# Kernel tuning notes

Measured on AMD Instinct MI355X. Metric: run time of the kernel, lower is better.

The kernel has to match this reference:

```python
import jax, jax.numpy as jnp
import numpy as np
from math import sqrt

N_HEADS = 8

def setup_inputs() -> dict:
    key = jax.random.key(0)
    k1, k2, k3 = jax.random.split(key, 3)
    B, S, D = 2, 2048, 512
    X = jax.random.normal(k1, (B, S, D), dtype=jnp.float32)
    # kaiming_normal for (fan_in = D) -> std = sqrt(2/D)
    Wq = jax.random.normal(k2, (D, D), dtype=jnp.float32) * jnp.float32(sqrt(2.0 / D))
    Wv = jax.random.normal(k3, (D, 1), dtype=jnp.float32) * jnp.float32(sqrt(2.0 / D))
    return {"X": X, "Wq": Wq, "Wv": Wv}

def reference(X, Wq, Wv):
    B, S, D = X.shape
    H = N_HEADS
    dh = D // H
    # Q: (B, H, S, dh)
    Q = (X @ Wq).reshape(B, S, H, dh).transpose(0, 2, 1, 3)
    # NOTE: original uses L2 norm (NOT squared) in the 'distance' expression; be faithful.
    n = jnp.linalg.norm(Q, axis=-1, keepdims=True)          # (B,H,S,1)
    dots = jnp.einsum('bhsd,bhtd->bhst', Q, Q)              # (B,H,S,S)
    scores = -(n - 2.0 * dots + jnp.swapaxes(n, -2, -1)) / jnp.float32(sqrt(dh))
    P = jax.nn.softmax(scores, axis=-1)                     # (B,H,S,S)
    # Wh: (H, D, dh); Ah = Wh @ Wh^T : (H, D, D)
    Wh = Wq.reshape(D, H, dh).transpose(1, 0, 2)
    Ah = jnp.einsum('hij,hkj->hik', Wh, Wh)
    PX = jnp.einsum('bhst,btd->bhsd', P, X)                 # (B,H,S,D)
    attn_scores = jnp.einsum('bhsd,hde->bhse', PX, Ah)      # (B,H,S,D)
    applied = attn_scores @ Wv                              # (B,H,S,1)
    # GumbelSigmoid in eval mode (deterministic): plain sigmoid of logits.
    selection = jax.nn.sigmoid(applied)
    return selection
```

## Files before the change

### kernel.cpp

```cpp
#include <hip/hip_runtime.h>


typedef __attribute__((ext_vector_type(8))) short bf16x8;
typedef __attribute__((ext_vector_type(4))) float f32x4;

#if __has_builtin(__builtin_amdgcn_exp2f)
#define EXP2F(x) __builtin_amdgcn_exp2f(x)
#else
#define EXP2F(x) exp2f(x)
#endif

#define LOG2E 1.44269504088896341f
#define C025  (0.25f * LOG2E)
#define C0125 (0.125f * LOG2E)

__device__ inline unsigned int f2b(float f) {
    unsigned int u = __float_as_uint(f);
    return (u + 0x7fffu + ((u >> 16) & 1u)) >> 16;
}

#define SWZ(row, c) ((row) * 64 + (((c) ^ ((row) & 7)) * 8))

__global__ __launch_bounds__(256) void qgemm_k(const float* __restrict__ X,
                                               const float* __restrict__ Wq,
                                               const float* __restrict__ Wv,
                                               unsigned short* __restrict__ Qh,
                                               float* __restrict__ n_out,
                                               float* __restrict__ y_out) {
    __shared__ __align__(16) unsigned short As[64 * 64];
    __shared__ __align__(16) unsigned short Bs[64 * 64];
    __shared__ float tsh[256];
    int tid = threadIdx.x;
    int h = blockIdx.x;
    int m0 = blockIdx.y * 64;
    int n0 = h * 64;
    int w = tid >> 6, lane = tid & 63;
    int tt = lane & 15, quad = lane >> 4;

    int arow = tid >> 3, achk = tid & 7;
    int bc = tid & 63, bjg = tid >> 6;

    const float* Xa0 = &X[(m0 + arow) * 512 + achk * 8];
    const float* Xa1 = Xa0 + 32 * 512;
    const float* Wb  = &Wq[n0 + bc];

    float4 a00, a01, a10, a11;
    float bv[16], wv[16];
    float tp = 0.f;
    f32x4 acc[4] = {{0.f,0.f,0.f,0.f},{0.f,0.f,0.f,0.f},
                    {0.f,0.f,0.f,0.f},{0.f,0.f,0.f,0.f}};

#define K1_LOADS(K0)                                                     \
    do {                                                                 \
        a00 = *(const float4*)&Xa0[(K0)];                                \
        a01 = *(const float4*)&Xa0[(K0) + 4];                            \
        a10 = *(const float4*)&Xa1[(K0)];                                \
        a11 = *(const float4*)&Xa1[(K0) + 4];                            \
        _Pragma("unroll")                                                \
        for (int i = 0; i < 8; ++i) {                                    \
            bv[i]     = Wb[((K0) + bjg * 8 + i) * 512];                  \
            bv[8 + i] = Wb[((K0) + (bjg + 4) * 8 + i) * 512];            \
            wv[i]     = Wv[(K0) + bjg * 8 + i];                          \
            wv[8 + i] = Wv[(K0) + (bjg + 4) * 8 + i];                    \
        }                                                                \
    } while (0)

    K1_LOADS(0);
    for (int k0 = 0; k0 < 512; k0 += 64) {
        __syncthreads();
        uint4 o;
        o.x = f2b(a00.x) | (f2b(a00.y) << 16);
        o.y = f2b(a00.z) | (f2b(a00.w) << 16);
        o.z = f2b(a01.x) | (f2b(a01.y) << 16);
        o.w = f2b(a01.z) | (f2b(a01.w) << 16);
        *(uint4*)&As[SWZ(arow, achk)] = o;
        o.x = f2b(a10.x) | (f2b(a10.y) << 16);
        o.y = f2b(a10.z) | (f2b(a10.w) << 16);
        o.z = f2b(a11.x) | (f2b(a11.y) << 16);
        o.w = f2b(a11.z) | (f2b(a11.w) << 16);
        *(uint4*)&As[SWZ(arow + 32, achk)] = o;
        o.x = f2b(bv[0]) | (f2b(bv[1]) << 16);
        o.y = f2b(bv[2]) | (f2b(bv[3]) << 16);
        o.z = f2b(bv[4]) | (f2b(bv[5]) << 16);
        o.w = f2b(bv[6]) | (f2b(bv[7]) << 16);
        *(uint4*)&Bs[SWZ(bc, bjg)] = o;
        o.x = f2b(bv[8])  | (f2b(bv[9])  << 16);
        o.y = f2b(bv[10]) | (f2b(bv[11]) << 16);
        o.z = f2b(bv[12]) | (f2b(bv[13]) << 16);
        o.w = f2b(bv[14]) | (f2b(bv[15]) << 16);
        *(uint4*)&Bs[SWZ(bc, bjg + 4)] = o;
        #pragma unroll
        for (int i = 0; i < 16; ++i) tp = fmaf(bv[i], wv[i], tp);
        __syncthreads();
        if (k0 < 448) K1_LOADS(k0 + 64);
        int ar = w * 16 + tt;
        bf16x8 fa0 = *(const bf16x8*)&As[SWZ(ar, quad)];
        bf16x8 fa1 = *(const bf16x8*)&As[SWZ(ar, quad + 4)];
        #pragma unroll
        for (int ct = 0; ct < 4; ++ct) {
            int br = ct * 16 + tt;
            bf16x8 fb0 = *(const bf16x8*)&Bs[SWZ(br, quad)];
            bf16x8 fb1 = *(const bf16x8*)&Bs[SWZ(br, quad + 4)];
            acc[ct] = __builtin_amdgcn_mfma_f32_16x16x32_bf16(fa0, fb0, acc[ct], 0, 0, 0);
            acc[ct] = __builtin_amdgcn_mfma_f32_16x16x32_bf16(fa1, fb1, acc[ct], 0, 0, 0);
        }
    }

    tsh[bjg * 64 + bc] = tp;
    __syncthreads();
    float tv[4];
    #pragma unroll
    for (int ct = 0; ct < 4; ++ct) {
        int c = ct * 16 + tt;
        tv[ct] = tsh[c] + tsh[64 + c] + tsh[128 + c] + tsh[192 + c];
    }

    float s2[4] = {0.f,0.f,0.f,0.f}, yp[4] = {0.f,0.f,0.f,0.f};
    #pragma unroll
    for (int ct = 0; ct < 4; ++ct)
        #pragma unroll
        for (int g = 0; g < 4; ++g) {
            float v = acc[ct][g];
            s2[g] = fmaf(v, v, s2[g]);
            yp[g] = fmaf(v, tv[ct], yp[g]);
            Qh[(m0 + w * 16 + quad * 4 + g) * 512 + n0 + ct * 16 + tt] =
                (unsigned short)f2b(v);
        }
    #pragma unroll
    for (int off = 1; off <= 8; off <<= 1)
        #pragma unroll
        for (int g = 0; g < 4; ++g) {
            s2[g] += __shfl_xor(s2[g], off);
            yp[g] += __shfl_xor(yp[g], off);
        }
    if (tt == 0) {
        int bb = m0 >> 11;
        #pragma unroll
        for (int g = 0; g < 4; ++g) {
            int row = m0 + w * 16 + quad * 4 + g;
            int idx = ((bb * 8 + h) << 11) + (row & 2047);
            n_out[idx] = sqrtf(s2[g]);
            y_out[idx] = yp[g];
        }
    }
}

__global__ __launch_bounds__(512, 4) void attn_k(const unsigned short* __restrict__ Qh,
                                                 const float* __restrict__ n_in,
                                                 const float* __restrict__ y_in,
                                                 float* __restrict__ out) {
    __shared__ float redN[8][64];
    __shared__ float redD[8][64];
    int tid = threadIdx.x;
    int bh = blockIdx.x >> 5;
    int tile = blockIdx.x & 31;
    int s0 = tile * 64;
    int b = bh >> 3, h = bh & 7;
    const unsigned short* Qb = Qh + (size_t)(b * 2048) * 512 + h * 64;
    const float* nb = n_in + bh * 2048;
    const float* yb = y_in + bh * 2048;
    int w = tid >> 6, lane = tid & 63;
    int tt = lane & 15, quad = lane >> 4;

    bf16x8 fa0[4], fa1[4];
    #pragma unroll
    for (int tl = 0; tl < 4; ++tl) {
        const unsigned short* r = &Qb[(size_t)(s0 + tl * 16 + tt) * 512];
        fa0[tl] = *(const bf16x8*)&r[quad * 8];
        fa1[tl] = *(const bf16x8*)&r[32 + quad * 8];
    }
    f32x4 num[4] = {{0.f,0.f,0.f,0.f},{0.f,0.f,0.f,0.f},
                    {0.f,0.f,0.f,0.f},{0.f,0.f,0.f,0.f}};
    f32x4 den[4] = {{0.f,0.f,0.f,0.f},{0.f,0.f,0.f,0.f},
                    {0.f,0.f,0.f,0.f},{0.f,0.f,0.f,0.f}};

    for (int st = 0; st < 16; ++st) {
        int tbase = w * 256 + st * 16;
        const unsigned short* rT = &Qb[(size_t)(tbase + tt) * 512];
        bf16x8 fb0 = *(const bf16x8*)&rT[quad * 8];
        bf16x8 fb1 = *(const bf16x8*)&rT[32 + quad * 8];
        float tqv = -C0125 * nb[tbase + tt];
        float yv  = yb[tbase + tt];
        #pragma unroll
        for (int tl = 0; tl < 4; ++tl) {
            f32x4 dot = {0.f, 0.f, 0.f, 0.f};
            dot = __builtin_amdgcn_mfma_f32_16x16x32_bf16(fa0[tl], fb0, dot, 0, 0, 0);
            dot = __builtin_amdgcn_mfma_f32_16x16x32_bf16(fa1[tl], fb1, dot, 0, 0, 0);
            #pragma unroll
            for (int g = 0; g < 4; ++g) {
                float arg = fmaf(C025, dot[g], tqv);
                float e = EXP2F(arg);
                num[tl][g] = fmaf(e, yv, num[tl][g]);
                den[tl][g] += e;
            }
        }
    }

    #pragma unroll
    for (int off = 1; off <= 8; off <<= 1)
        #pragma unroll
        for (int tl = 0; tl < 4; ++tl)
            #pragma unroll
            for (int g = 0; g < 4; ++g) {
                num[tl][g] += __shfl_xor(num[tl][g], off);
                den[tl][g] += __shfl_xor(den[tl][g], off);
            }
    if (tt == 0) {
        #pragma unroll
        for (int tl = 0; tl < 4; ++tl)
            #pragma unroll
            for (int g = 0; g < 4; ++g) {
                redN[w][tl * 16 + quad * 4 + g] = num[tl][g];
                redD[w][tl * 16 + quad * 4 + g] = den[tl][g];
            }
    }
    __syncthreads();
    if (tid < 64) {
        float xn = 0.f, xd = 0.f;
        #pragma unroll
        for (int ww = 0; ww < 8; ++ww) {
            xn += redN[ww][tid];
            xd += redD[ww][tid];
        }
        float x = xn / xd;
        out[bh * 2048 + s0 + tid] = 1.0f / (1.0f + EXP2F(-x * LOG2E));
    }
}

extern "C" void kernel_launch(void* const* d_in, const int* in_sizes, int n_in,
                              void* d_out, int out_size, void* d_ws, size_t ws_size,
                              hipStream_t stream) {
    const float* X  = (const float*)d_in[0];
    const float* Wq = (const float*)d_in[1];
    const float* Wv = (const float*)d_in[2];
    float* ws = (float*)d_ws;

    float* n_ws = ws;
    float* y_ws = ws + 32768;
    unsigned short* Qh_ws = (unsigned short*)(ws + 65536);

    qgemm_k<<<dim3(8, 64), 256, 0, stream>>>(X, Wq, Wv, Qh_ws, n_ws, y_ws);
    attn_k<<<512, 512, 0, stream>>>(Qh_ws, n_ws, y_ws, (float*)d_out);
}
```

Baseline: 99.35 us.

## Fuse Q-projection GEMM and attention into one kernel with per-head counters

Merges the Q-projection GEMM kernel and the attention kernel into a single 512-block launch. Each block first computes a 64x64 Q tile with 8 waves split as 4 row groups by 2 column groups. It then signals a per-(batch,head) atomic counter and spins until all 32 tiles for its head are written before running the attention pass. This removes the second launch and the gap between kernels, and it prescales the norm term once in the GEMM epilogue. In exchange it adds a memset launch and a spin barrier that depends on all 512 blocks being co-resident; if they are not, the kernel can deadlock.

```diff
diff --git a/kernel.cpp b/kernel.cpp
--- a/kernel.cpp
+++ b/kernel.cpp
@@ -21,209 +21,218 @@
 
 #define SWZ(row, c) ((row) * 64 + (((c) ^ ((row) & 7)) * 8))
 
-__global__ __launch_bounds__(256) void qgemm_k(const float* __restrict__ X,
-                                               const float* __restrict__ Wq,
-                                               const float* __restrict__ Wv,
-                                               unsigned short* __restrict__ Qh,
-                                               float* __restrict__ n_out,
-                                               float* __restrict__ y_out) {
+__global__ __launch_bounds__(512, 4) void fused_k(const float* __restrict__ X,
+                                                  const float* __restrict__ Wq,
+                                                  const float* __restrict__ Wv,
+                                                  unsigned short* __restrict__ Qh,
+                                                  float* __restrict__ nl_ws,
+                                                  float* __restrict__ y_ws,
+                                                  unsigned int* __restrict__ cnt,
+                                                  float* __restrict__ out) {
     __shared__ __align__(16) unsigned short As[64 * 64];
     __shared__ __align__(16) unsigned short Bs[64 * 64];
-    __shared__ float tsh[256];
+    __shared__ float tsh[512];
+    __shared__ float redS[2][64], redY[2][64];
+    __shared__ float redN[8][64], redD[8][64];
+
     int tid = threadIdx.x;
-    int h = blockIdx.x;
-    int m0 = blockIdx.y * 64;
-    int n0 = h * 64;
+    int bid = blockIdx.x;
     int w = tid >> 6, lane = tid & 63;
     int tt = lane & 15, quad = lane >> 4;
 
-    int arow = tid >> 3, achk = tid & 7;
-    int bc = tid & 63, bjg = tid >> 6;
-
-    const float* Xa0 = &X[(m0 + arow) * 512 + achk * 8];
-    const float* Xa1 = Xa0 + 32 * 512;
-    const float* Wb  = &Wq[n0 + bc];
-
-    float4 a00, a01, a10, a11;
-    float bv[16], wv[16];
-    float tp = 0.f;
-    f32x4 acc[4] = {{0.f,0.f,0.f,0.f},{0.f,0.f,0.f,0.f},
-                    {0.f,0.f,0.f,0.f},{0.f,0.f,0.f,0.f}};
-
-#define K1_LOADS(K0)                                                     \
-    do {                                                                 \
-        a00 = *(const float4*)&Xa0[(K0)];                                \
-        a01 = *(const float4*)&Xa0[(K0) + 4];                            \
-        a10 = *(const float4*)&Xa1[(K0)];                                \
-        a11 = *(const float4*)&Xa1[(K0) + 4];                            \
-        _Pragma("unroll")                                                \
-        for (int i = 0; i < 8; ++i) {                                    \
-            bv[i]     = Wb[((K0) + bjg * 8 + i) * 512];                  \
-            bv[8 + i] = Wb[((K0) + (bjg + 4) * 8 + i) * 512];            \
-            wv[i]     = Wv[(K0) + bjg * 8 + i];                          \
-            wv[8 + i] = Wv[(K0) + (bjg + 4) * 8 + i];                    \
-        }                                                                \
-    } while (0)
-
-    K1_LOADS(0);
-    for (int k0 = 0; k0 < 512; k0 += 64) {
-        __syncthreads();
-        uint4 o;
-        o.x = f2b(a00.x) | (f2b(a00.y) << 16);
-        o.y = f2b(a00.z) | (f2b(a00.w) << 16);
-        o.z = f2b(a01.x) | (f2b(a01.y) << 16);
-        o.w = f2b(a01.z) | (f2b(a01.w) << 16);
-        *(uint4*)&As[SWZ(arow, achk)] = o;
-        o.x = f2b(a10.x) | (f2b(a10.y) << 16);
-        o.y = f2b(a10.z) | (f2b(a10.w) << 16);
-        o.z = f2b(a11.x) | (f2b(a11.y) << 16);
-        o.w = f2b(a11.z) | (f2b(a11.w) << 16);
-        *(uint4*)&As[SWZ(arow + 32, achk)] = o;
-        o.x = f2b(bv[0]) | (f2b(bv[1]) << 16);
-        o.y = f2b(bv[2]) | (f2b(bv[3]) << 16);
-        o.z = f2b(bv[4]) | (f2b(bv[5]) << 16);
-        o.w = f2b(bv[6]) | (f2b(bv[7]) << 16);
-        *(uint4*)&Bs[SWZ(bc, bjg)] = o;
-        o.x = f2b(bv[8])  | (f2b(bv[9])  << 16);
-        o.y = f2b(bv[10]) | (f2b(bv[11]) << 16);
-        o.z = f2b(bv[12]) | (f2b(bv[13]) << 16);
-        o.w = f2b(bv[14]) | (f2b(bv[15]) << 16);
-        *(uint4*)&Bs[SWZ(bc, bjg + 4)] = o;
-        #pragma unroll
-        for (int i = 0; i < 16; ++i) tp = fmaf(bv[i], wv[i], tp);
-        __syncthreads();
-        if (k0 < 448) K1_LOADS(k0 + 64);
-        int ar = w * 16 + tt;
-        bf16x8 fa0 = *(const bf16x8*)&As[SWZ(ar, quad)];
-        bf16x8 fa1 = *(const bf16x8*)&As[SWZ(ar, quad + 4)];
-        #pragma unroll
-        for (int ct = 0; ct < 4; ++ct) {
-            int br = ct * 16 + tt;
-            bf16x8 fb0 = *(const bf16x8*)&Bs[SWZ(br, quad)];
-            bf16x8 fb1 = *(const bf16x8*)&Bs[SWZ(br, quad + 4)];
-            acc[ct] = __builtin_amdgcn_mfma_f32_16x16x32_bf16(fa0, fb0, acc[ct], 0, 0, 0);
-            acc[ct] = __builtin_amdgcn_mfma_f32_16x16x32_bf16(fa1, fb1, acc[ct], 0, 0, 0);
+    {
+        int h = bid & 7;
+        int m0 = (bid >> 3) * 64;
+        int n0 = h * 64;
+        int rg = w >> 1, cg = w & 1;
+
+        int arow = tid >> 3, achk = tid & 7;
+        int bc = tid & 63, bjg = tid >> 6;
+
+        const float* Xa = &X[(m0 + arow) * 512 + achk * 8];
+        const float* Wb = &Wq[n0 + bc];
+
+        float4 a0v, a1v;
+        float bv[8], wvv[8];
+        float tp = 0.f;
+        f32x4 acc[2] = {{0.f,0.f,0.f,0.f},{0.f,0.f,0.f,0.f}};
+
+#define LOADS(K0)                                                    \
+        do {                                                         \
+            a0v = *(const float4*)&Xa[(K0)];                         \
+            a1v = *(const float4*)&Xa[(K0) + 4];                     \
+            _Pragma("unroll")                                        \
+            for (int i = 0; i < 8; ++i) {                            \
+                bv[i]  = Wb[((K0) + bjg * 8 + i) * 512];             \
+                wvv[i] = Wv[(K0) + bjg * 8 + i];                     \
+            }                                                        \
+        } while (0)
+
+        LOADS(0);
+        for (int k0 = 0; k0 < 512; k0 += 64) {
+            __syncthreads();
+            uint4 o;
+            o.x = f2b(a0v.x) | (f2b(a0v.y) << 16);
+            o.y = f2b(a0v.z) | (f2b(a0v.w) << 16);
+            o.z = f2b(a1v.x) | (f2b(a1v.y) << 16);
+            o.w = f2b(a1v.z) | (f2b(a1v.w) << 16);
+            *(uint4*)&As[SWZ(arow, achk)] = o;
+            o.x = f2b(bv[0]) | (f2b(bv[1]) << 16);
+            o.y = f2b(bv[2]) | (f2b(bv[3]) << 16);
+            o.z = f2b(bv[4]) | (f2b(bv[5]) << 16);
+            o.w = f2b(bv[6]) | (f2b(bv[7]) << 16);
+            *(uint4*)&Bs[SWZ(bc, bjg)] = o;
+            #pragma unroll
+            for (int i = 0; i < 8; ++i) tp = fmaf(bv[i], wvv[i], tp);
+            __syncthreads();
+            if (k0 < 448) LOADS(k0 + 64);
+            int ar = rg * 16 + tt;
+            bf16x8 fa0 = *(const bf16x8*)&As[SWZ(ar, quad)];
+            bf16x8 fa1 = *(const bf16x8*)&As[SWZ(ar, quad + 4)];
+            #pragma unroll
+            for (int c = 0; c < 2; ++c) {
+                int br = (cg * 2 + c) * 16 + tt;
+                bf16x8 fb0 = *(const bf16x8*)&Bs[SWZ(br, quad)];
+                bf16x8 fb1 = *(const bf16x8*)&Bs[SWZ(br, quad + 4)];
+                acc[c] = __builtin_amdgcn_mfma_f32_16x16x32_bf16(fa0, fb0, acc[c], 0, 0, 0);
+                acc[c] = __builtin_amdgcn_mfma_f32_16x16x32_bf16(fa1, fb1, acc[c], 0, 0, 0);
+            }
+        }
+
+        tsh[bjg * 64 + bc] = tp;
+        __syncthreads();
+        float tv[2];
+        #pragma unroll
+        for (int c = 0; c < 2; ++c) {
+            int col = (cg * 2 + c) * 16 + tt;
+            float s = 0.f;
+            #pragma unroll
+            for (int j = 0; j < 8; ++j) s += tsh[j * 64 + col];
+            tv[c] = s;
+        }
+
+        float s2[4] = {0.f,0.f,0.f,0.f}, yp[4] = {0.f,0.f,0.f,0.f};
+        #pragma unroll
+        for (int c = 0; c < 2; ++c)
+            #pragma unroll
+            for (int g = 0; g < 4; ++g) {
+                float v = acc[c][g];
+                s2[g] = fmaf(v, v, s2[g]);
+                yp[g] = fmaf(v, tv[c], yp[g]);
+                Qh[(m0 + rg * 16 + quad * 4 + g) * 512 + n0 + (cg * 2 + c) * 16 + tt] =
+                    (unsigned short)f2b(v);
+            }
+        #pragma unroll
+        for (int off = 1; off <= 8; off <<= 1)
+            #pragma unroll
+            for (int g = 0; g < 4; ++g) {
+                s2[g] += __shfl_xor(s2[g], off);
+                yp[g] += __shfl_xor(yp[g], off);
+            }
+        if (tt == 0) {
+            #pragma unroll
+            for (int g = 0; g < 4; ++g) {
+                redS[cg][rg * 16 + quad * 4 + g] = s2[g];
+                redY[cg][rg * 16 + quad * 4 + g] = yp[g];
+            }
+        }
+        __syncthreads();
+        if (tid < 64) {
+            float s = redS[0][tid] + redS[1][tid];
+            float y = redY[0][tid] + redY[1][tid];
+            int bb = m0 >> 11;
+            int idx = ((bb * 8 + h) << 11) + ((m0 + tid) & 2047);
+            nl_ws[idx] = -C0125 * sqrtf(s);
+            y_ws[idx] = y;
         }
     }
 
-    tsh[bjg * 64 + bc] = tp;
-    __syncthreads();
-    float tv[4];
-    #pragma unroll
-    for (int ct = 0; ct < 4; ++ct) {
-        int c = ct * 16 + tt;
-        tv[ct] = tsh[c] + tsh[64 + c] + tsh[128 + c] + tsh[192 + c];
+    {
+        int g1 = (bid >> 8) * 8 + (bid & 7);
+        int bh2 = bid >> 5;
+        __syncthreads();
+        __threadfence();
+        if (tid == 0) {
+            atomicAdd(&cnt[g1], 1u);
+            while (atomicAdd(&cnt[bh2], 0u) < 32u)
+                __builtin_amdgcn_s_sleep(4);
+        }
+        __syncthreads();
+        __threadfence();
     }
 
-    float s2[4] = {0.f,0.f,0.f,0.f}, yp[4] = {0.f,0.f,0.f,0.f};
-    #pragma unroll
-    for (int ct = 0; ct < 4; ++ct)
-        #pragma unroll
-        for (int g = 0; g < 4; ++g) {
-            float v = acc[ct][g];
-            s2[g] = fmaf(v, v, s2[g]);
-            yp[g] = fmaf(v, tv[ct], yp[g]);
-            Qh[(m0 + w * 16 + quad * 4 + g) * 512 + n0 + ct * 16 + tt] =
-                (unsigned short)f2b(v);
-        }
-    #pragma unroll
-    for (int off = 1; off <= 8; off <<= 1)
-        #pragma unroll
-        for (int g = 0; g < 4; ++g) {
-            s2[g] += __shfl_xor(s2[g], off);
-            yp[g] += __shfl_xor(yp[g], off);
-        }
-    if (tt == 0) {
-        int bb = m0 >> 11;
-        #pragma unroll
-        for (int g = 0; g < 4; ++g) {
-            int row = m0 + w * 16 + quad * 4 + g;
-            int idx = ((bb * 8 + h) << 11) + (row & 2047);
-            n_out[idx] = sqrtf(s2[g]);
-            y_out[idx] = yp[g];
-        }
-    }
-}
-
-__global__ __launch_bounds__(512, 4) void attn_k(const unsigned short* __restrict__ Qh,
-                                                 const float* __restrict__ n_in,
-                                                 const float* __restrict__ y_in,
-                                                 float* __restrict__ out) {
-    __shared__ float redN[8][64];
-    __shared__ float redD[8][64];
-    int tid = threadIdx.x;
-    int bh = blockIdx.x >> 5;
-    int tile = blockIdx.x & 31;
-    int s0 = tile * 64;
-    int b = bh >> 3, h = bh & 7;
-    const unsigned short* Qb = Qh + (size_t)(b * 2048) * 512 + h * 64;
-    const float* nb = n_in + bh * 2048;
-    const float* yb = y_in + bh * 2048;
-    int w = tid >> 6, lane = tid & 63;
-    int tt = lane & 15, quad = lane >> 4;
-
-    bf16x8 fa0[4], fa1[4];
-    #pragma unroll
-    for (int tl = 0; tl < 4; ++tl) {
-        const unsigned short* r = &Qb[(size_t)(s0 + tl * 16 + tt) * 512];
-        fa0[tl] = *(const bf16x8*)&r[quad * 8];
-        fa1[tl] = *(const bf16x8*)&r[32 + quad * 8];
-    }
-    f32x4 num[4] = {{0.f,0.f,0.f,0.f},{0.f,0.f,0.f,0.f},
-                    {0.f,0.f,0.f,0.f},{0.f,0.f,0.f,0.f}};
-    f32x4 den[4] = {{0.f,0.f,0.f,0.f},{0.f,0.f,0.f,0.f},
-                    {0.f,0.f,0.f,0.f},{0.f,0.f,0.f,0.f}};
-
-    for (int st = 0; st < 16; ++st) {
-        int tbase = w * 256 + st * 16;
-        const unsigned short* rT = &Qb[(size_t)(tbase + tt) * 512];
-        bf16x8 fb0 = *(const bf16x8*)&rT[quad * 8];
-        bf16x8 fb1 = *(const bf16x8*)&rT[32 + quad * 8];
-        float tqv = -C0125 * nb[tbase + tt];
-        float yv  = yb[tbase + tt];
+    {
+        int bh = bid >> 5;
+        int tile = bid & 31;
+        int s0 = tile * 64;
+        int b = bh >> 3, h = bh & 7;
+        const unsigned short* Qb = Qh + (size_t)(b * 2048) * 512 + h * 64;
+        const float* nb = nl_ws + bh * 2048;
+        const float* yb = y_ws + bh * 2048;
+
+        bf16x8 fa0[4], fa1[4];
         #pragma unroll
         for (int tl = 0; tl < 4; ++tl) {
-            f32x4 dot = {0.f, 0.f, 0.f, 0.f};
-            dot = __builtin_amdgcn_mfma_f32_16x16x32_bf16(fa0[tl], fb0, dot, 0, 0, 0);
-            dot = __builtin_amdgcn_mfma_f32_16x16x32_bf16(fa1[tl], fb1, dot, 0, 0, 0);
-            #pragma unroll
-            for (int g = 0; g < 4; ++g) {
-                float arg = fmaf(C025, dot[g], tqv);
-                float e = EXP2F(arg);
-                num[tl][g] = fmaf(e, yv, num[tl][g]);
-                den[tl][g] += e;
-            }
-        }
-    }
-
-    #pragma unroll
-    for (int off = 1; off <= 8; off <<= 1)
-        #pragma unroll
-        for (int tl = 0; tl < 4; ++tl)
-            #pragma unroll
-            for (int g = 0; g < 4; ++g) {
-                num[tl][g] += __shfl_xor(num[tl][g], off);
-                den[tl][g] += __shfl_xor(den[tl][g], off);
-            }
-    if (tt == 0) {
-        #pragma unroll
-        for (int tl = 0; tl < 4; ++tl)
-            #pragma unroll
-            for (int g = 0; g < 4; ++g) {
-                redN[w][tl * 16 + quad * 4 + g] = num[tl][g];
-                redD[w][tl * 16 + quad * 4 + g] = den[tl][g];
-            }
-    }
-    __syncthreads();
-    if (tid < 64) {
-        float xn = 0.f, xd = 0.f;
-        #pragma unroll
-        for (int ww = 0; ww < 8; ++ww) {
-            xn += redN[ww][tid];
-            xd += redD[ww][tid];
-        }
-        float x = xn / xd;
-        out[bh * 2048 + s0 + tid] = 1.0f / (1.0f + EXP2F(-x * LOG2E));
+            const unsigned short* r = &Qb[(size_t)(s0 + tl * 16 + tt) * 512];
+            fa0[tl] = *(const bf16x8*)&r[quad * 8];
+            fa1[tl] = *(const bf16x8*)&r[32 + quad * 8];
+        }
+        f32x4 num[4] = {{0.f,0.f,0.f,0.f},{0.f,0.f,0.f,0.f},
+                        {0.f,0.f,0.f,0.f},{0.f,0.f,0.f,0.f}};
+        f32x4 den[4] = {{0.f,0.f,0.f,0.f},{0.f,0.f,0.f,0.f},
+                        {0.f,0.f,0.f,0.f},{0.f,0.f,0.f,0.f}};
+
+        for (int st = 0; st < 16; ++st) {
+            int tbase = w * 256 + st * 16;
+            const unsigned short* rT = &Qb[(size_t)(tbase + tt) * 512];
+            bf16x8 fb0 = *(const bf16x8*)&rT[quad * 8];
+            bf16x8 fb1 = *(const bf16x8*)&rT[32 + quad * 8];
+            float tqv = nb[tbase + tt];
+            float yv  = yb[tbase + tt];
+            #pragma unroll
+            for (int tl = 0; tl < 4; ++tl) {
+                f32x4 dot = {0.f, 0.f, 0.f, 0.f};
+                dot = __builtin_amdgcn_mfma_f32_16x16x32_bf16(fa0[tl], fb0, dot, 0, 0, 0);
+                dot = __builtin_amdgcn_mfma_f32_16x16x32_bf16(fa1[tl], fb1, dot, 0, 0, 0);
+                #pragma unroll
+                for (int g = 0; g < 4; ++g) {
+                    float arg = fmaf(C025, dot[g], tqv);
+                    float e = EXP2F(arg);
+                    num[tl][g] = fmaf(e, yv, num[tl][g]);
+                    den[tl][g] += e;
+                }
+            }
+        }
+
+        #pragma unroll
+        for (int off = 1; off <= 8; off <<= 1)
+            #pragma unroll
+            for (int tl = 0; tl < 4; ++tl)
+                #pragma unroll
+                for (int g = 0; g < 4; ++g) {
+                    num[tl][g] += __shfl_xor(num[tl][g], off);
+                    den[tl][g] += __shfl_xor(den[tl][g], off);
+                }
+        if (tt == 0) {
+            #pragma unroll
+            for (int tl = 0; tl < 4; ++tl)
+                #pragma unroll
+                for (int g = 0; g < 4; ++g) {
+                    redN[w][tl * 16 + quad * 4 + g] = num[tl][g];
+                    redD[w][tl * 16 + quad * 4 + g] = den[tl][g];
+                }
+        }
+        __syncthreads();
+        if (tid < 64) {
+            float xn = 0.f, xd = 0.f;
+            #pragma unroll
+            for (int ww = 0; ww < 8; ++ww) {
+                xn += redN[ww][tid];
+                xd += redD[ww][tid];
+            }
+            float x = xn / xd;
+            out[bh * 2048 + s0 + tid] = 1.0f / (1.0f + EXP2F(-x * LOG2E));
+        }
     }
 }
 
@@ -233,12 +242,14 @@
     const float* X  = (const float*)d_in[0];
     const float* Wq = (const float*)d_in[1];
     const float* Wv = (const float*)d_in[2];
+    float* outp = (float*)d_out;
     float* ws = (float*)d_ws;
 
-    float* n_ws = ws;
-    float* y_ws = ws + 32768;
-    unsigned short* Qh_ws = (unsigned short*)(ws + 65536);
-
-    qgemm_k<<<dim3(8, 64), 256, 0, stream>>>(X, Wq, Wv, Qh_ws, n_ws, y_ws);
-    attn_k<<<512, 512, 0, stream>>>(Qh_ws, n_ws, y_ws, (float*)d_out);
+    float* nl_ws = ws;
+    float* y_ws  = ws + 32768;
+    unsigned int* cnt_ws = (unsigned int*)(ws + 65536);
+    unsigned short* Qh_ws = (unsigned short*)(ws + 65552);
+
+    hipMemsetAsync(cnt_ws, 0, 64, stream);
+    fused_k<<<512, 512, 0, stream>>>(X, Wq, Wv, Qh_ws, nl_ws, y_ws, cnt_ws, outp);
 }
```

New measurement: 261.9 us. 164% more time.
